# Performance work log

Hardware: AMD Instinct MI355X
Metric: run time of the kernel (lower is better)

Reference implementation:

```python
import jax, jax.numpy as jnp
import numpy as np

N_PRED = 10000
N_GT = 1000
NUM_CLASSES = 80
IMG_H = 800
IMG_W = 1333
EPS = 1e-12
ALPHA, GAMMA, CLS_W = 0.25, 2.0, 2.0
L1_W, IOU_W = 5.0, 2.0
CENTER_RADIUS = 2.5
CAND_TOPK = 5


def _make_boxes(key, n, w, h):
    k1, k2 = jax.random.split(key)
    cxcy = jax.random.uniform(k1, (n, 2)) * jnp.array([w, h], jnp.float32)
    wh = jax.random.uniform(k2, (n, 2)) * 190.0 + 10.0
    return jnp.concatenate([cxcy - wh / 2, cxcy + wh / 2], axis=1).astype(jnp.float32)


def setup_inputs() -> dict:
    key = jax.random.key(0)
    k1, k2, k3, k4 = jax.random.split(key, 4)
    return {
        'pred_logits': jax.random.normal(k1, (N_PRED, NUM_CLASSES), jnp.float32),
        'pred_boxes': _make_boxes(k2, N_PRED, IMG_W, IMG_H),
        'gt_bboxes': _make_boxes(k3, N_GT, IMG_W, IMG_H),
        'gt_labels': jax.random.randint(k4, (N_GT,), 0, NUM_CLASSES),
        'img_h': IMG_H,
        'img_w': IMG_W,
    }


def _pairwise_iou_giou(pred, gt):
    area_p = (pred[:, 2] - pred[:, 0]) * (pred[:, 3] - pred[:, 1])
    area_g = (gt[:, 2] - gt[:, 0]) * (gt[:, 3] - gt[:, 1])
    lt = jnp.maximum(pred[:, None, :2], gt[None, :, :2])
    rb = jnp.minimum(pred[:, None, 2:], gt[None, :, 2:])
    wh = jnp.clip(rb - lt, 0.0)
    inter = wh[..., 0] * wh[..., 1]                       # [N,G]
    union = area_p[:, None] + area_g[None, :] - inter
    iou = inter / jnp.maximum(union, EPS)
    elt = jnp.minimum(pred[:, None, :2], gt[None, :, :2])
    erb = jnp.maximum(pred[:, None, 2:], gt[None, :, 2:])
    ewh = jnp.clip(erb - elt, 0.0)
    enclose = ewh[..., 0] * ewh[..., 1]
    giou = iou - (enclose - union) / jnp.maximum(enclose, EPS)
    return iou, giou


def _center_info(pred, gt):
    # pred/gt in xyxy; uses pred box centers, strict inequalities as in source
    pcx = (pred[:, 0] + pred[:, 2]) * 0.5
    pcy = (pred[:, 1] + pred[:, 3]) * 0.5
    gx1, gy1, gx2, gy2 = gt[:, 0], gt[:, 1], gt[:, 2], gt[:, 3]
    in_boxes = ((pcx[:, None] > gx1) & (pcx[:, None] < gx2) &
                (pcy[:, None] > gy1) & (pcy[:, None] < gy2))
    gcx, gcy = (gx1 + gx2) * 0.5, (gy1 + gy2) * 0.5
    gw, gh = gx2 - gx1, gy2 - gy1
    r = CENTER_RADIUS
    in_centers = ((pcx[:, None] > gcx - r * gw) & (pcx[:, None] < gcx + r * gw) &
                  (pcy[:, None] > gcy - r * gh) & (pcy[:, None] < gcy + r * gh))
    valid = in_boxes.any(1) | in_centers.any(1)
    return valid, in_boxes & in_centers


def _compute_cost_and_ious(pred_logits, pred_boxes, gt_bboxes, gt_labels, img_h, img_w):
    # FocalLossCost
    p = jax.nn.sigmoid(pred_logits)
    neg = -jnp.log1p(-(p - EPS)) * (1 - ALPHA) * p ** GAMMA
    pos = -jnp.log(p + EPS) * ALPHA * (1 - p) ** GAMMA
    cls_cost = (pos - neg)[:, gt_labels] * CLS_W            # [N,G]
    # BBoxL1Cost (normalized by image size)
    factor = jnp.array([img_w, img_h, img_w, img_h], jnp.float32)
    l1_cost = jnp.sum(jnp.abs(pred_boxes[:, None, :] / factor -
                              gt_bboxes[None, :, :] / factor), -1) * L1_W
    # IoUCost (giou) + pairwise ious for dynamic-k
    ious, giou = _pairwise_iou_giou(pred_boxes, gt_bboxes)
    iou_cost = -giou * IOU_W
    valid_mask, in_boxes_and_center = _center_info(pred_boxes, gt_bboxes)
    cost = cls_cost + l1_cost + iou_cost + jnp.where(in_boxes_and_center, 0.0, 100.0)
    cost = cost + jnp.where(valid_mask, 0.0, 10000.0)[:, None]
    return cost, ious


def _dynamic_k_matching(cost, ious):
    n, g = cost.shape
    k = min(CAND_TOPK, n)
    topk_ious, _ = jax.lax.top_k(ious.T, k)                 # [G,k]
    dynamic_ks = jnp.maximum(topk_ious.sum(1).astype(jnp.int32), 1)
    _, idx = jax.lax.top_k(-cost.T, k)                      # [G,k] smallest costs per gt
    vals = (jnp.arange(k)[None, :] < dynamic_ks[:, None]).astype(cost.dtype)
    cols = jnp.broadcast_to(jnp.arange(g)[:, None], (g, k))
    mm = jnp.zeros_like(cost).at[idx, cols].max(vals)       # scatter 1s per gt column
    # resolve priors matched to >1 gt (note: mask is reused stale inside the loop, as in source)
    prior_mask = mm.sum(1) > 1
    cmin = jnp.argmin(cost, axis=1)
    mm = jnp.where(prior_mask[:, None], jax.nn.one_hot(cmin, g, dtype=cost.dtype), mm)

    def cond(state):
        m, _ = state
        return jnp.any(m.sum(0) == 0)

    def body(state):
        m, c = state
        matched_q = m.sum(1) > 0
        c = c + 100000.0 * matched_q[:, None].astype(c.dtype)
        unmatched = m.sum(0) == 0
        pos = jnp.argmin(c, axis=0)                         # [G]
        oh = jax.nn.one_hot(pos, n, dtype=c.dtype).T        # [N,G]
        m = jnp.where(unmatched[None, :], oh, m)
        cmin2 = jnp.argmin(c, axis=1)
        m_fix = jnp.where(prior_mask[:, None], jax.nn.one_hot(cmin2, g, dtype=c.dtype), m)
        m = jnp.where(jnp.any(m.sum(1) > 1), m_fix, m)
        return (m, c)

    mm, _ = jax.lax.while_loop(cond, body, (mm, cost))
    fg_mask = mm.sum(1) > 0
    matched = jnp.argmax(mm, axis=1).astype(jnp.int32)
    return fg_mask, jnp.where(fg_mask, matched, 0)


def reference(pred_logits, pred_boxes, gt_bboxes, gt_labels, img_h, img_w):
    cost, ious = _compute_cost_and_ious(pred_logits, pred_boxes, gt_bboxes,
                                        gt_labels, img_h, img_w)
    fg_mask, matched_gt = _dynamic_k_matching(cost, ious)
    # dense form: matched_gt[i] valid only where fg_mask[i] (fixed-shape version of
    # the original's compressed matched_gt_inds = mm[fg_mask].argmax(1))
    return fg_mask, matched_gt
```

## Files before the change

kernel.cpp:

```cpp
#include <hip/hip_runtime.h>
#include <cfloat>
#include <cmath>

#define NP 10000
#define NG 1000
#define NC 80
#define LMAX 6
#define NCH 4
#define CHSZ (NP / NCH)
#define CMAIN 9
#define CTAIL 196

#define S_MULTI 12
#define S_BODY  16
#define RI_BIG  0x3fffffff
#define KMAX    0xFFFFFFFFFFFFFFFFull

#define TKEY    0xC248000000000000ull

#define WCAP    448

__device__ __forceinline__ bool lexless(float av, int ai, float bv, int bi) {
    return (av < bv) || (av == bv && ai < bi);
}

__device__ __forceinline__ unsigned long long packkey(float v, int idx) {
    unsigned u = __float_as_uint(v);
    u ^= (unsigned)(((int)u) >> 31) | 0x80000000u;
    return ((unsigned long long)u << 32) | (unsigned)idx;
}
__device__ __forceinline__ int keyidx(unsigned long long k) {
    return (int)(unsigned)(k & 0xFFFFFFFFu);
}

__device__ __forceinline__ float inflate(float c, int k) {
    for (int q = 0; q < k; q++) c += 100000.0f;
    return c;
}

__device__ __forceinline__ void cost_iou(float4 p, float4 pn, float4 pi,
        float4 g, float4 cb, float4 Gn, float ga, float clsv,
        float& cc_out, float& iou_out) {
#pragma clang fp contract(off)
    float wx = fminf(p.z, g.z) - fmaxf(p.x, g.x); wx = fmaxf(wx, 0.0f);
    float wy = fminf(p.w, g.w) - fmaxf(p.y, g.y); wy = fmaxf(wy, 0.0f);
    float inter = wx * wy;
    float uni = pi.z + ga - inter;
    float iou = inter / fmaxf(uni, 1e-12f);
    float ex = fmaxf(p.z, g.z) - fminf(p.x, g.x); ex = fmaxf(ex, 0.0f);
    float ey = fmaxf(p.w, g.w) - fminf(p.y, g.y); ey = fmaxf(ey, 0.0f);
    float enc = ex * ey;
    float giou = iou - (enc - uni) / fmaxf(enc, 1e-12f);
    float l1 = ((fabsf(pn.x - Gn.x) + fabsf(pn.y - Gn.y))
                + fabsf(pn.z - Gn.z)) + fabsf(pn.w - Gn.w);
    float cc = clsv + l1 * 5.0f;
    cc = cc + (-giou * 2.0f);
    bool inb = (pi.x > g.x && pi.x < g.z && pi.y > g.y && pi.y < g.w);
    bool inc = (pi.x > cb.x && pi.x < cb.z && pi.y > cb.y && pi.y < cb.w);
    cc = cc + ((inb && inc) ? 0.0f : 100.0f);
    cc = cc + pi.w;
    cc_out = cc; iou_out = iou;
}

__device__ __forceinline__ void ins5k(unsigned long long* kv,
        unsigned long long key) {
    if (key < kv[4]) {
        kv[4] = key;
#pragma unroll
        for (int t = 4; t > 0; t--)
            if (kv[t] < kv[t-1]) { unsigned long long tv = kv[t]; kv[t] = kv[t-1]; kv[t-1] = tv; }
    }
}
__device__ __forceinline__ void ins5i(float* iv, float iou) {
    if (iou > iv[4]) {
        iv[4] = iou;
#pragma unroll
        for (int t = 4; t > 0; t--)
            if (iv[t] > iv[t-1]) { float tv = iv[t]; iv[t] = iv[t-1]; iv[t-1] = tv; }
    }
}

#define CLS_TI 64
#define PB_CLS0 40
#define PB_G0   197
#define PB_V0   201
__global__ __launch_bounds__(256) void k_prep(const float* __restrict__ logits,
        const float* __restrict__ pb, const float* __restrict__ gb,
        const int* __restrict__ imgw, const int* __restrict__ imgh,
        float* __restrict__ clsval, float4* __restrict__ pnorm,
        float4* __restrict__ pinfo, float4* __restrict__ gcb,
        float4* __restrict__ gnm, float* __restrict__ gar,
        int* rowcnt, int* rowfirst, int* rowiter, int* prior, int* priorcol,
        int* colsum, int* scal)
{
    __shared__ float sl[CLS_TI * (NC + 1)];
    int b = blockIdx.x;
    if (b < PB_CLS0) {
        int i = b * 256 + threadIdx.x;
        if (i < NP) {
            rowcnt[i] = 0; rowfirst[i] = 0x7fffffff; rowiter[i] = RI_BIG;
            prior[i] = 0; priorcol[i] = 0;
        }
        if (i < NG) colsum[i] = 0;
        if (i < 32) scal[i] = 0;
    } else if (b < PB_G0) {
        int i0 = (b - PB_CLS0) * CLS_TI;
        bool full = (i0 + CLS_TI) <= NP;
        if (full) {
            const float* src = logits + (size_t)i0 * NC;
            for (int e = threadIdx.x; e < CLS_TI * NC; e += 256) {
                int di = e / NC, c = e - di * NC;
                sl[di * (NC + 1) + c] = src[e];
            }
        } else {
            for (int e = threadIdx.x; e < CLS_TI * NC; e += 256) {
                int di = e / NC, c = e - di * NC;
                int i = i0 + di;
                sl[di * (NC + 1) + c] = (i < NP) ? logits[(size_t)i * NC + c] : 0.0f;
            }
        }
        __syncthreads();
        for (int e = threadIdx.x; e < CLS_TI * NC; e += 256) {
            int c = e >> 6, di = e & 63;
            int i = i0 + di;
            if (i >= NP) continue;
            float x = sl[di * (NC + 1) + c];
            float p = 1.0f / (1.0f + expf(-x));
            float neg = -log1pf(-(p - 1e-12f)) * 0.75f * (p * p);
            float om = 1.0f - p;
            float pos = -logf(p + 1e-12f) * 0.25f * (om * om);
            clsval[(size_t)c * NP + i] = (pos - neg) * 2.0f;
        }
    } else if (b < PB_V0) {
#pragma clang fp contract(off)
        int j = (b - PB_G0) * 256 + threadIdx.x;
        if (j < NG) {
            float fw = (float)imgw[0], fh = (float)imgh[0];
            float4 g = ((const float4*)gb)[j];
            float gcx = (g.x + g.z) * 0.5f, gcy = (g.y + g.w) * 0.5f;
            float gw = g.z - g.x, gh = g.w - g.y;
            float4 cb; cb.x = gcx - 2.5f * gw; cb.y = gcy - 2.5f * gh;
            cb.z = gcx + 2.5f * gw; cb.w = gcy + 2.5f * gh;
            gcb[j] = cb;
            float4 Gn; Gn.x = g.x / fw; Gn.y = g.y / fh; Gn.z = g.z / fw; Gn.w = g.w / fh;
            gnm[j] = Gn;
            gar[j] = (g.z - g.x) * (g.w - g.y);
        }
    } else {
#pragma clang fp contract(off)
        int wave = threadIdx.x >> 6;
        int lane = threadIdx.x & 63;
        int i = (b - PB_V0) * 4 + wave;
        if (i >= NP) return;
        float4 p = ((const float4*)pb)[i];
        float pcx = (p.x + p.z) * 0.5f, pcy = (p.y + p.w) * 0.5f;
        int vb = 0, vc = 0;
        const float4* gb4 = (const float4*)gb;
        for (int jb = 0; jb < NG; jb += 64) {
            int j = jb + lane;
            if (j < NG) {
                float4 g = gb4[j];
                vb |= (pcx > g.x && pcx < g.z && pcy > g.y && pcy < g.w) ? 1 : 0;
                float gcx = (g.x + g.z) * 0.5f, gcy = (g.y + g.w) * 0.5f;
                float gw = g.z - g.x, gh = g.w - g.y;
                vc |= (pcx > gcx - 2.5f * gw && pcx < gcx + 2.5f * gw &&
                       pcy > gcy - 2.5f * gh && pcy < gcy + 2.5f * gh) ? 1 : 0;
            }
            if (__any(vb | vc)) break;
        }
        int any = __any(vb | vc) ? 1 : 0;
        if (lane == 0) {
            float fw = (float)imgw[0], fh = (float)imgh[0];
            float4 pn; pn.x = p.x / fw; pn.y = p.y / fh; pn.z = p.z / fw; pn.w = p.w / fh;
            pnorm[i] = pn;
            float4 pi4; pi4.x = pcx; pi4.y = pcy;
            pi4.z = (p.z - p.x) * (p.w - p.y);
            pi4.w = any ? 0.0f : 10000.0f;
            pinfo[i] = pi4;
        }
    }
}

__device__ __forceinline__ void tree57(unsigned long long* s_k, float* s_iv,
        int tid) {
    for (int w = 128; w > 0; w >>= 1) {
        if (tid < w) {
            int a = tid * 7, bb = (tid + w) * 7;
            unsigned long long ok[5]; float og[5];
            int pa = a, pbp = bb;
#pragma unroll
            for (int t = 0; t < 5; t++) {
                unsigned long long A = s_k[pa], B = s_k[pbp];
                if (A <= B) { ok[t] = A; pa++; } else { ok[t] = B; pbp++; }
            }
            int qa = a, qb = bb;
#pragma unroll
            for (int t = 0; t < 5; t++) {
                float A = s_iv[qa], B = s_iv[qb];
                if (A >= B) { og[t] = A; qa++; } else { og[t] = B; qb++; }
            }
#pragma unroll
            for (int t = 0; t < 5; t++) { s_k[a+t] = ok[t]; s_iv[a+t] = og[t]; }
        }
        __syncthreads();
    }
}

__global__ __launch_bounds__(256) void k_cost2(
        const float* __restrict__ pb, const float* __restrict__ gb,
        const int* __restrict__ glab, const float* __restrict__ clsval,
        const float4* __restrict__ pnorm, const float4* __restrict__ pinfo,
        const float4* __restrict__ gcb, const float4* __restrict__ gnm,
        const float* __restrict__ gar,
        unsigned long long* __restrict__ pck, float* __restrict__ piv)
{
    __shared__ unsigned long long s_k[256 * 7];
    __shared__ float s_iv[256 * 7];
    __shared__ int s_wcnt[4];
    int* s_list = (int*)s_iv;

    int j = blockIdx.x >> 2;
    int c = blockIdx.x & 3;
    int tid = threadIdx.x;
    int wid = tid >> 6;
    int ln  = tid & 63;
    float4 g  = ((const float4*)gb)[j];
    float4 cb = gcb[j];
    float4 Gn = gnm[j];
    float  ga = gar[j];
    const float* clscol = clsval + (size_t)glab[j] * NP;
    const float4* pb4 = (const float4*)pb;
    int base_i = c * CHSZ;

    int wbase = 0;
    for (int k = 0; k <= CMAIN; k++) {
        if (k == CMAIN && tid >= CTAIL) break;
        int i = base_i + tid + k * 256;
        float4 p = pb4[i];
        bool o = (p.z > g.x) & (g.z > p.x) & (p.w > g.y) & (g.w > p.y);
        unsigned long long m = __ballot(o ? 1 : 0);
        if (o) {
            int slot = wbase + __popcll(m & ((1ull << ln) - 1ull));
            if (slot < WCAP) s_list[wid * WCAP + slot] = i;
        }
        wbase += __popcll(m);
    }
    if (ln == 0) s_wcnt[wid] = wbase;
    __syncthreads();
    int c0 = s_wcnt[0], c1 = s_wcnt[1], c2 = s_wcnt[2], c3 = s_wcnt[3];
    bool overflow = (c0 > WCAP) | (c1 > WCAP) | (c2 > WCAP) | (c3 > WCAP);

    unsigned long long kv[5]; float iv[5];
#pragma unroll
    for (int t = 0; t < 5; t++) { kv[t] = KMAX; iv[t] = overflow ? -1.0f : 0.0f; }

    if (!overflow) {
        for (int q = tid; q < c0; q += 256) {
            int i = s_list[q];
            float cc, iou;
            cost_iou(pb4[i], pnorm[i], pinfo[i], g, cb, Gn, ga, clscol[i], cc, iou);
            ins5k(kv, packkey(cc, i)); ins5i(iv, iou);
        }
        for (int q = tid; q < c1; q += 256) {
            int i = s_list[WCAP + q];
            float cc, iou;
            cost_iou(pb4[i], pnorm[i], pinfo[i], g, cb, Gn, ga, clscol[i], cc, iou);
            ins5k(kv, packkey(cc, i)); ins5i(iv, iou);
        }
        for (int q = tid; q < c2; q += 256) {
            int i = s_list[2 * WCAP + q];
            float cc, iou;
            cost_iou(pb4[i], pnorm[i], pinfo[i], g, cb, Gn, ga, clscol[i], cc, iou);
            ins5k(kv, packkey(cc, i)); ins5i(iv, iou);
        }
        for (int q = tid; q < c3; q += 256) {
            int i = s_list[3 * WCAP + q];
            float cc, iou;
            cost_iou(pb4[i], pnorm[i], pinfo[i], g, cb, Gn, ga, clscol[i], cc, iou);
            ins5k(kv, packkey(cc, i)); ins5i(iv, iou);
        }
    } else {
        for (int k = 0; k <= CMAIN; k++) {
            if (k == CMAIN && tid >= CTAIL) break;
            int i = base_i + tid + k * 256;
            float cc, iou;
            cost_iou(pb4[i], pnorm[i], pinfo[i], g, cb, Gn, ga, clscol[i], cc, iou);
            ins5k(kv, packkey(cc, i)); ins5i(iv, iou);
        }
    }
    __syncthreads();

    int base = tid * 7;
#pragma unroll
    for (int t = 0; t < 5; t++) { s_k[base+t] = kv[t]; s_iv[base+t] = iv[t]; }
    s_k[base+5] = KMAX; s_iv[base+5] = -2.0f;
    __syncthreads();
    tree57(s_k, s_iv, tid);

    bool redo = !overflow && (s_k[4] >= TKEY);
    __syncthreads();

    if (redo) {
#pragma unroll
        for (int t = 0; t < 5; t++) { kv[t] = KMAX; iv[t] = -1.0f; }
        for (int k = 0; k <= CMAIN; k++) {
            if (k == CMAIN && tid >= CTAIL) break;
            int i = base_i + tid + k * 256;
            float cc, iou;
            cost_iou(pb4[i], pnorm[i], pinfo[i], g, cb, Gn, ga, clscol[i], cc, iou);
            ins5k(kv, packkey(cc, i)); ins5i(iv, iou);
        }
#pragma unroll
        for (int t = 0; t < 5; t++) { s_k[base+t] = kv[t]; s_iv[base+t] = iv[t]; }
        s_k[base+5] = KMAX; s_iv[base+5] = -2.0f;
        __syncthreads();
        tree57(s_k, s_iv, tid);
    }

    if (tid == 0) {
        int ob = blockIdx.x * 5;
#pragma unroll
        for (int t = 0; t < 5; t++) { pck[ob + t] = s_k[t]; piv[ob + t] = s_iv[t]; }
    }
}

__global__ __launch_bounds__(256) void k_costmerge(
        const unsigned long long* __restrict__ pck, const float* __restrict__ piv,
        int* __restrict__ rowcnt, int* __restrict__ rowfirst,
        int* __restrict__ rowiter, int* __restrict__ top5,
        int* __restrict__ dkarr)
{
    int j = blockIdx.x * 256 + threadIdx.x;
    if (j >= NG) return;
    int base = j * NCH * 5;
    int h0 = 0, h1 = 0, h2 = 0, h3 = 0;
    int besti[5];
#pragma unroll
    for (int r = 0; r < 5; r++) {
        unsigned long long v0 = (h0 < 5) ? pck[base + h0]      : KMAX;
        unsigned long long v1 = (h1 < 5) ? pck[base + 5 + h1]  : KMAX;
        unsigned long long v2 = (h2 < 5) ? pck[base + 10 + h2] : KMAX;
        unsigned long long v3 = (h3 < 5) ? pck[base + 15 + h3] : KMAX;
        unsigned long long best = v0; int sel = 0;
        if (v1 < best) { best = v1; sel = 1; }
        if (v2 < best) { best = v2; sel = 2; }
        if (v3 < best) { best = v3; sel = 3; }
        besti[r] = keyidx(best);
        h0 += (sel == 0); h1 += (sel == 1); h2 += (sel == 2); h3 += (sel == 3);
    }
    int g0 = 0, g1 = 0, g2 = 0, g3 = 0;
    float ivm[5];
#pragma unroll
    for (int r = 0; r < 5; r++) {
        float w0 = (g0 < 5) ? piv[base + g0]      : -2.0f;
        float w1 = (g1 < 5) ? piv[base + 5 + g1]  : -2.0f;
        float w2 = (g2 < 5) ? piv[base + 10 + g2] : -2.0f;
        float w3 = (g3 < 5) ? piv[base + 15 + g3] : -2.0f;
        float best = w0; int sel = 0;
        if (w1 > best) { best = w1; sel = 1; }
        if (w2 > best) { best = w2; sel = 2; }
        if (w3 > best) { best = w3; sel = 3; }
        ivm[r] = best;
        g0 += (sel == 0); g1 += (sel == 1); g2 += (sel == 2); g3 += (sel == 3);
    }
    float s = (((ivm[0] + ivm[1]) + ivm[2]) + ivm[3]) + ivm[4];
    int dk = (int)s;
    if (dk < 1) dk = 1;
    dkarr[j] = dk;
#pragma unroll
    for (int r = 0; r < 5; r++) top5[j * 5 + r] = besti[r];
    for (int t = 0; t < dk; t++) {
        int r = besti[t];
        atomicAdd(&rowcnt[r], 1);
        atomicMin(&rowfirst[r], j);
        atomicMin(&rowiter[r], -1);
    }
}

__global__ __launch_bounds__(256) void k_pfixsurv(const float* __restrict__ pb,
        const float* __restrict__ gb, const int* __restrict__ glab,
        const float* __restrict__ clsval,
        const float4* __restrict__ pnorm, const float4* __restrict__ pinfo,
        const float4* __restrict__ gcb, const float4* __restrict__ gnm,
        const float* __restrict__ gar,
        int* __restrict__ prior, int* __restrict__ priorcol,
        int* __restrict__ colsum,
        const int* __restrict__ rowcnt, const int* __restrict__ top5,
        const int* __restrict__ dkarr)
{
    int b = blockIdx.x;
    int tid = threadIdx.x;
    if (b >= 2500) {
        int j = (b - 2500) * 256 + tid;
        if (j >= NG) return;
        int c = 0;
        int dk = dkarr[j];
        for (int t = 0; t < dk; t++) if (rowcnt[top5[j * 5 + t]] == 1) c++;
        if (c) atomicAdd(&colsum[j], c);
        return;
    }
    __shared__ float rv[256]; __shared__ int ri[256];
    for (int q = 0; q < 4; q++) {
        int row = b * 4 + q;
        if (rowcnt[row] <= 1) continue;
        if (tid == 0) prior[row] = 1;
        float4 p = ((const float4*)pb)[row];
        float4 pn = pnorm[row];
        float4 pi4 = pinfo[row];
        float best = FLT_MAX; int bj = 0x7fffffff;
        for (int j = tid; j < NG; j += 256) {
            float cc, iou;
            cost_iou(p, pn, pi4, ((const float4*)gb)[j], gcb[j], gnm[j], gar[j],
                     clsval[(size_t)glab[j] * NP + row], cc, iou);
            if (lexless(cc, j, best, bj)) { best = cc; bj = j; }
        }
        rv[tid] = best; ri[tid] = bj; __syncthreads();
        for (int w = 128; w > 0; w >>= 1) {
            if (tid < w) {
                float ov = rv[tid + w]; int oi = ri[tid + w];
                if (lexless(ov, oi, rv[tid], ri[tid])) { rv[tid] = ov; ri[tid] = oi; }
            }
            __syncthreads();
        }
        if (tid == 0) {
            priorcol[row] = ri[0];
            atomicAdd(&colsum[ri[0]], 1);
        }
        __syncthreads();
    }
}

__global__ __launch_bounds__(256) void k_iterB(const float* __restrict__ pb,
        const float* __restrict__ gb, const int* __restrict__ glab,
        const float* __restrict__ clsval,
        const float4* __restrict__ pnorm, const float4* __restrict__ pinfo,
        const float4* __restrict__ gcb, const float4* __restrict__ gnm,
        const float* __restrict__ gar, const int* __restrict__ top5,
        int* __restrict__ rowiter, int* __restrict__ rowcnt,
        int* __restrict__ rowfirst, int* __restrict__ colsum,
        int* __restrict__ scal, int t)
{
    int j = blockIdx.x;
    if (colsum[j] != 0) return;
    int tid = threadIdx.x;
    if (tid == 0) scal[S_BODY + t] = 1;

    __shared__ int s_pos;
    if (tid == 0) {
        int pos = -1;
        for (int r = 0; r < 5; r++) {
            int i = top5[j * 5 + r];
            if (rowiter[i] >= t) { pos = i; break; }
        }
        s_pos = pos;
    }
    __syncthreads();
    int pos = s_pos;

    if (pos < 0) {
        float4 g  = ((const float4*)gb)[j];
        float4 cb = gcb[j];
        float4 Gn = gnm[j];
        float  ga = gar[j];
        const float* clscol = clsval + (size_t)glab[j] * NP;
        const float4* pb4 = (const float4*)pb;
        __shared__ float rv[256]; __shared__ int ri[256];
        float best = FLT_MAX; int bi = 0x7fffffff;
        for (int i = tid; i < NP; i += 256) {
            if (rowiter[i] < t) continue;
            float cc, iou;
            cost_iou(pb4[i], pnorm[i], pinfo[i], g, cb, Gn, ga, clscol[i], cc, iou);
            if (lexless(cc, i, best, bi)) { best = cc; bi = i; }
        }
        rv[tid] = best; ri[tid] = bi; __syncthreads();
        for (int w = 128; w > 0; w >>= 1) {
            if (tid < w) {
                float ov = rv[tid + w]; int oi = ri[tid + w];
                if (lexless(ov, oi, rv[tid], ri[tid])) { rv[tid] = ov; ri[tid] = oi; }
            }
            __syncthreads();
        }
        pos = ri[0];
    }

    if (tid == 0) {
        colsum[j] = 1;
        int old = atomicAdd(&rowcnt[pos], 1);
        if (old >= 1) scal[S_MULTI] = 1;
        atomicMin(&rowfirst[pos], j);
        atomicMin(&rowiter[pos], t);
    }
}

__global__ __launch_bounds__(256) void k_iterC(const float* __restrict__ pb,
        const float* __restrict__ gb, const int* __restrict__ glab,
        const float* __restrict__ clsval,
        const float4* __restrict__ pnorm, const float4* __restrict__ pinfo,
        const float4* __restrict__ gcb, const float4* __restrict__ gnm,
        const float* __restrict__ gar,
        const int* __restrict__ prior, const int* __restrict__ rowiter,
        int* __restrict__ priorcol, int* __restrict__ colsum,
        int* __restrict__ scal, int t)
{
    if (scal[S_BODY + t] == 0 || scal[S_MULTI] == 0) return;
    int b = blockIdx.x;
    int tid = threadIdx.x;
    __shared__ float rv[256]; __shared__ int ri[256];
    for (int q = 0; q < 4; q++) {
        int row = b * 4 + q;
        if (!prior[row]) continue;
        int k = t - rowiter[row]; if (k < 0) k = 0;
        float4 p = ((const float4*)pb)[row];
        float4 pn = pnorm[row];
        float4 pi4 = pinfo[row];
        float best = FLT_MAX; int bj = 0x7fffffff;
        for (int j = tid; j < NG; j += 256) {
            float cc, iou;
            cost_iou(p, pn, pi4, ((const float4*)gb)[j], gcb[j], gnm[j], gar[j],
                     clsval[(size_t)glab[j] * NP + row], cc, iou);
            float val = inflate(cc, k);
            if (lexless(val, j, best, bj)) { best = val; bj = j; }
        }
        rv[tid] = best; ri[tid] = bj; __syncthreads();
        for (int w = 128; w > 0; w >>= 1) {
            if (tid < w) {
                float ov = rv[tid + w]; int oi = ri[tid + w];
                if (lexless(ov, oi, rv[tid], ri[tid])) { rv[tid] = ov; ri[tid] = oi; }
            }
            __syncthreads();
        }
        if (tid == 0) {
            int nb = ri[0];
            int oldc = priorcol[row];
            if (nb != oldc) {
                atomicSub(&colsum[oldc], 1);
                atomicAdd(&colsum[nb], 1);
                priorcol[row] = nb;
            }
        }
        __syncthreads();
    }
}

__global__ __launch_bounds__(256) void k_final(const int* __restrict__ rowcnt,
        const int* __restrict__ prior, const int* __restrict__ priorcol,
        const int* __restrict__ rowfirst, int* __restrict__ out)
{
    int i = blockIdx.x * 256 + threadIdx.x;
    if (i >= NP) return;
    int fg = rowcnt[i] > 0;
    out[i] = fg ? 1 : 0;
    out[NP + i] = fg ? (prior[i] ? priorcol[i] : rowfirst[i]) : 0;
}

extern "C" void kernel_launch(void* const* d_in, const int* in_sizes, int n_in,
                              void* d_out, int out_size, void* d_ws, size_t ws_size,
                              hipStream_t stream)
{
    (void)in_sizes; (void)n_in; (void)out_size; (void)ws_size;
    const float* logits = (const float*)d_in[0];
    const float* pboxes = (const float*)d_in[1];
    const float* gboxes = (const float*)d_in[2];
    const int*   glab   = (const int*)d_in[3];
    const int*   imgh   = (const int*)d_in[4];
    const int*   imgw   = (const int*)d_in[5];
    int* out = (int*)d_out;

    char* w = (char*)d_ws;
    float*  clsval  = (float*)(w);
    float4* pnorm   = (float4*)(w + 3200000);
    float4* pinfo   = (float4*)(w + 3360000);
    float4* gcb     = (float4*)(w + 3520000);
    float4* gnm     = (float4*)(w + 3536000);
    float*  gar     = (float*)(w + 3552000);
    int* rowcnt     = (int*)(w + 3556000);
    int* rowfirst   = (int*)(w + 3596000);
    int* rowiter    = (int*)(w + 3636000);
    int* prior      = (int*)(w + 3676000);
    int* priorcol   = (int*)(w + 3716000);
    int* top5       = (int*)(w + 3756000);
    int* dkarr      = (int*)(w + 3776000);
    int* colsum     = (int*)(w + 3780000);
    int* scal       = (int*)(w + 3784000);
    unsigned long long* pck = (unsigned long long*)(w + 3784128);
    float* piv      = (float*)(w + 3944128);

    hipLaunchKernelGGL(k_prep, dim3(2701), dim3(256), 0, stream,
                       logits, pboxes, gboxes, imgw, imgh,
                       clsval, pnorm, pinfo, gcb, gnm, gar,
                       rowcnt, rowfirst, rowiter, prior, priorcol, colsum, scal);
    hipLaunchKernelGGL(k_cost2, dim3(NG * NCH), dim3(256), 0, stream,
                       pboxes, gboxes, glab, clsval, pnorm, pinfo, gcb, gnm, gar,
                       pck, piv);
    hipLaunchKernelGGL(k_costmerge, dim3(4), dim3(256), 0, stream,
                       pck, piv, rowcnt, rowfirst, rowiter, top5, dkarr);
    hipLaunchKernelGGL(k_pfixsurv, dim3(2504), dim3(256), 0, stream,
                       pboxes, gboxes, glab, clsval, pnorm, pinfo, gcb, gnm, gar,
                       prior, priorcol, colsum, rowcnt, top5, dkarr);
    for (int t = 0; t < LMAX; t++) {
        hipLaunchKernelGGL(k_iterB, dim3(NG), dim3(256), 0, stream,
                           pboxes, gboxes, glab, clsval, pnorm, pinfo, gcb, gnm, gar,
                           top5, rowiter, rowcnt, rowfirst, colsum, scal, t);
        hipLaunchKernelGGL(k_iterC, dim3(2500), dim3(256), 0, stream,
                           pboxes, gboxes, glab, clsval, pnorm, pinfo, gcb, gnm, gar,
                           prior, rowiter, priorcol, colsum, scal, t);
    }
    hipLaunchKernelGGL(k_final, dim3(40), dim3(256), 0, stream,
                       rowcnt, prior, priorcol, rowfirst, out);
}
```

Measured before the change: 163.1 us.

## Assign each wave one prediction chunk and merge top-5 via wave shuffles

The cost kernel now launches one block per ground-truth box, and each of the four waves independently handles one quarter of the predictions. This replaces the four-blocks-per-GT scheme. The shared-memory tree merge with many __syncthreads is replaced by a butterfly shuffle merge of sorted top-5 lists within each wave, and the per-wave candidate list capacity is raised. The intent is to remove block-wide barriers and shared-memory traffic. In exchange, each wave scans four times as many boxes serially and the grid has fewer blocks.

```diff
diff --git a/kernel.cpp b/kernel.cpp
--- a/kernel.cpp
+++ b/kernel.cpp
@@ -8,8 +8,8 @@
 #define LMAX 6
 #define NCH 4
 #define CHSZ (NP / NCH)
-#define CMAIN 9
-#define CTAIL 196
+#define WMAIN 39
+#define WTAIL 4
 
 #define S_MULTI 12
 #define S_BODY  16
@@ -18,7 +18,7 @@
 
 #define TKEY    0xC248000000000000ull
 
-#define WCAP    448
+#define WCAP    768
 
 __device__ __forceinline__ bool lexless(float av, int ai, float bv, int bi) {
     return (av < bv) || (av == bv && ai < bi);
@@ -80,6 +80,55 @@
     }
 }
 
+__device__ __forceinline__ void cswapk(unsigned long long& a,
+        unsigned long long& b) {
+    unsigned long long lo = (a < b) ? a : b;
+    unsigned long long hi = (a < b) ? b : a;
+    a = lo; b = hi;
+}
+__device__ __forceinline__ void sort5k(unsigned long long* a) {
+    cswapk(a[0],a[1]); cswapk(a[3],a[4]); cswapk(a[2],a[4]);
+    cswapk(a[2],a[3]); cswapk(a[1],a[4]); cswapk(a[0],a[3]);
+    cswapk(a[0],a[2]); cswapk(a[1],a[3]); cswapk(a[1],a[2]);
+}
+__device__ __forceinline__ void cswapi(float& a, float& b) {
+    float hi = fmaxf(a, b), lo = fminf(a, b);
+    a = hi; b = lo;
+}
+__device__ __forceinline__ void sort5i(float* a) {
+    cswapi(a[0],a[1]); cswapi(a[3],a[4]); cswapi(a[2],a[4]);
+    cswapi(a[2],a[3]); cswapi(a[1],a[4]); cswapi(a[0],a[3]);
+    cswapi(a[0],a[2]); cswapi(a[1],a[3]); cswapi(a[1],a[2]);
+}
+
+__device__ __forceinline__ void wavemerge5(unsigned long long* kv, float* iv) {
+#pragma unroll
+    for (int d = 1; d < 64; d <<= 1) {
+        unsigned long long r0 = __shfl_xor(kv[0], d);
+        unsigned long long r1 = __shfl_xor(kv[1], d);
+        unsigned long long r2 = __shfl_xor(kv[2], d);
+        unsigned long long r3 = __shfl_xor(kv[3], d);
+        unsigned long long r4 = __shfl_xor(kv[4], d);
+        kv[0] = (kv[0] < r4) ? kv[0] : r4;
+        kv[1] = (kv[1] < r3) ? kv[1] : r3;
+        kv[2] = (kv[2] < r2) ? kv[2] : r2;
+        kv[3] = (kv[3] < r1) ? kv[3] : r1;
+        kv[4] = (kv[4] < r0) ? kv[4] : r0;
+        sort5k(kv);
+        float s0 = __shfl_xor(iv[0], d);
+        float s1 = __shfl_xor(iv[1], d);
+        float s2 = __shfl_xor(iv[2], d);
+        float s3 = __shfl_xor(iv[3], d);
+        float s4 = __shfl_xor(iv[4], d);
+        iv[0] = fmaxf(iv[0], s4);
+        iv[1] = fmaxf(iv[1], s3);
+        iv[2] = fmaxf(iv[2], s2);
+        iv[3] = fmaxf(iv[3], s1);
+        iv[4] = fmaxf(iv[4], s0);
+        sort5i(iv);
+    }
+}
+
 #define CLS_TI 64
 #define PB_CLS0 40
 #define PB_G0   197
@@ -181,31 +230,6 @@
     }
 }
 
-__device__ __forceinline__ void tree57(unsigned long long* s_k, float* s_iv,
-        int tid) {
-    for (int w = 128; w > 0; w >>= 1) {
-        if (tid < w) {
-            int a = tid * 7, bb = (tid + w) * 7;
-            unsigned long long ok[5]; float og[5];
-            int pa = a, pbp = bb;
-#pragma unroll
-            for (int t = 0; t < 5; t++) {
-                unsigned long long A = s_k[pa], B = s_k[pbp];
-                if (A <= B) { ok[t] = A; pa++; } else { ok[t] = B; pbp++; }
-            }
-            int qa = a, qb = bb;
-#pragma unroll
-            for (int t = 0; t < 5; t++) {
-                float A = s_iv[qa], B = s_iv[qb];
-                if (A >= B) { og[t] = A; qa++; } else { og[t] = B; qb++; }
-            }
-#pragma unroll
-            for (int t = 0; t < 5; t++) { s_k[a+t] = ok[t]; s_iv[a+t] = og[t]; }
-        }
-        __syncthreads();
-    }
-}
-
 __global__ __launch_bounds__(256) void k_cost2(
         const float* __restrict__ pb, const float* __restrict__ gb,
         const int* __restrict__ glab, const float* __restrict__ clsval,
@@ -214,13 +238,9 @@
         const float* __restrict__ gar,
         unsigned long long* __restrict__ pck, float* __restrict__ piv)
 {
-    __shared__ unsigned long long s_k[256 * 7];
-    __shared__ float s_iv[256 * 7];
-    __shared__ int s_wcnt[4];
-    int* s_list = (int*)s_iv;
-
-    int j = blockIdx.x >> 2;
-    int c = blockIdx.x & 3;
+    __shared__ int s_list[4 * WCAP];
+
+    int j = blockIdx.x;
     int tid = threadIdx.x;
     int wid = tid >> 6;
     int ln  = tid & 63;
@@ -230,14 +250,14 @@
     float  ga = gar[j];
     const float* clscol = clsval + (size_t)glab[j] * NP;
     const float4* pb4 = (const float4*)pb;
-    int base_i = c * CHSZ;
+    int base_i = wid * CHSZ;
 
     int wbase = 0;
-    for (int k = 0; k <= CMAIN; k++) {
-        if (k == CMAIN && tid >= CTAIL) break;
-        int i = base_i + tid + k * 256;
-        float4 p = pb4[i];
-        bool o = (p.z > g.x) & (g.z > p.x) & (p.w > g.y) & (g.w > p.y);
+    for (int k = 0; k <= WMAIN; k++) {
+        bool valid = (k < WMAIN) | (ln < WTAIL);
+        int i = base_i + ln + k * 64;
+        float4 p = pb4[valid ? i : base_i];
+        bool o = valid & (p.z > g.x) & (g.z > p.x) & (p.w > g.y) & (g.w > p.y);
         unsigned long long m = __ballot(o ? 1 : 0);
         if (o) {
             int slot = wbase + __popcll(m & ((1ull << ln) - 1ull));
@@ -245,82 +265,53 @@
         }
         wbase += __popcll(m);
     }
-    if (ln == 0) s_wcnt[wid] = wbase;
-    __syncthreads();
-    int c0 = s_wcnt[0], c1 = s_wcnt[1], c2 = s_wcnt[2], c3 = s_wcnt[3];
-    bool overflow = (c0 > WCAP) | (c1 > WCAP) | (c2 > WCAP) | (c3 > WCAP);
+    int cnt = wbase;
+    bool overflow = (cnt > WCAP);
 
     unsigned long long kv[5]; float iv[5];
 #pragma unroll
     for (int t = 0; t < 5; t++) { kv[t] = KMAX; iv[t] = overflow ? -1.0f : 0.0f; }
 
     if (!overflow) {
-        for (int q = tid; q < c0; q += 256) {
-            int i = s_list[q];
+        for (int q = ln; q < cnt; q += 64) {
+            int i = s_list[wid * WCAP + q];
             float cc, iou;
             cost_iou(pb4[i], pnorm[i], pinfo[i], g, cb, Gn, ga, clscol[i], cc, iou);
             ins5k(kv, packkey(cc, i)); ins5i(iv, iou);
         }
-        for (int q = tid; q < c1; q += 256) {
-            int i = s_list[WCAP + q];
-            float cc, iou;
-            cost_iou(pb4[i], pnorm[i], pinfo[i], g, cb, Gn, ga, clscol[i], cc, iou);
-            ins5k(kv, packkey(cc, i)); ins5i(iv, iou);
-        }
-        for (int q = tid; q < c2; q += 256) {
-            int i = s_list[2 * WCAP + q];
-            float cc, iou;
-            cost_iou(pb4[i], pnorm[i], pinfo[i], g, cb, Gn, ga, clscol[i], cc, iou);
-            ins5k(kv, packkey(cc, i)); ins5i(iv, iou);
-        }
-        for (int q = tid; q < c3; q += 256) {
-            int i = s_list[3 * WCAP + q];
-            float cc, iou;
-            cost_iou(pb4[i], pnorm[i], pinfo[i], g, cb, Gn, ga, clscol[i], cc, iou);
-            ins5k(kv, packkey(cc, i)); ins5i(iv, iou);
-        }
     } else {
-        for (int k = 0; k <= CMAIN; k++) {
-            if (k == CMAIN && tid >= CTAIL) break;
-            int i = base_i + tid + k * 256;
-            float cc, iou;
-            cost_iou(pb4[i], pnorm[i], pinfo[i], g, cb, Gn, ga, clscol[i], cc, iou);
-            ins5k(kv, packkey(cc, i)); ins5i(iv, iou);
-        }
-    }
-    __syncthreads();
-
-    int base = tid * 7;
-#pragma unroll
-    for (int t = 0; t < 5; t++) { s_k[base+t] = kv[t]; s_iv[base+t] = iv[t]; }
-    s_k[base+5] = KMAX; s_iv[base+5] = -2.0f;
-    __syncthreads();
-    tree57(s_k, s_iv, tid);
-
-    bool redo = !overflow && (s_k[4] >= TKEY);
-    __syncthreads();
-
+        for (int k = 0; k <= WMAIN; k++) {
+            bool valid = (k < WMAIN) | (ln < WTAIL);
+            if (valid) {
+                int i = base_i + ln + k * 64;
+                float cc, iou;
+                cost_iou(pb4[i], pnorm[i], pinfo[i], g, cb, Gn, ga, clscol[i], cc, iou);
+                ins5k(kv, packkey(cc, i)); ins5i(iv, iou);
+            }
+        }
+    }
+    wavemerge5(kv, iv);
+
+    bool redo = !overflow && (kv[4] >= TKEY);
     if (redo) {
 #pragma unroll
         for (int t = 0; t < 5; t++) { kv[t] = KMAX; iv[t] = -1.0f; }
-        for (int k = 0; k <= CMAIN; k++) {
-            if (k == CMAIN && tid >= CTAIL) break;
-            int i = base_i + tid + k * 256;
-            float cc, iou;
-            cost_iou(pb4[i], pnorm[i], pinfo[i], g, cb, Gn, ga, clscol[i], cc, iou);
-            ins5k(kv, packkey(cc, i)); ins5i(iv, iou);
-        }
-#pragma unroll
-        for (int t = 0; t < 5; t++) { s_k[base+t] = kv[t]; s_iv[base+t] = iv[t]; }
-        s_k[base+5] = KMAX; s_iv[base+5] = -2.0f;
-        __syncthreads();
-        tree57(s_k, s_iv, tid);
-    }
-
-    if (tid == 0) {
-        int ob = blockIdx.x * 5;
-#pragma unroll
-        for (int t = 0; t < 5; t++) { pck[ob + t] = s_k[t]; piv[ob + t] = s_iv[t]; }
+        for (int k = 0; k <= WMAIN; k++) {
+            bool valid = (k < WMAIN) | (ln < WTAIL);
+            if (valid) {
+                int i = base_i + ln + k * 64;
+                float cc, iou;
+                cost_iou(pb4[i], pnorm[i], pinfo[i], g, cb, Gn, ga, clscol[i], cc, iou);
+                ins5k(kv, packkey(cc, i)); ins5i(iv, iou);
+            }
+        }
+        wavemerge5(kv, iv);
+    }
+
+    if (ln == 0) {
+        int ob = (j * NCH + wid) * 5;
+#pragma unroll
+        for (int t = 0; t < 5; t++) { pck[ob + t] = kv[t]; piv[ob + t] = iv[t]; }
     }
 }
 
@@ -589,7 +580,7 @@
                        logits, pboxes, gboxes, imgw, imgh,
                        clsval, pnorm, pinfo, gcb, gnm, gar,
                        rowcnt, rowfirst, rowiter, prior, priorcol, colsum, scal);
-    hipLaunchKernelGGL(k_cost2, dim3(NG * NCH), dim3(256), 0, stream,
+    hipLaunchKernelGGL(k_cost2, dim3(NG), dim3(256), 0, stream,
                        pboxes, gboxes, glab, clsval, pnorm, pinfo, gcb, gnm, gar,
                        pck, piv);
     hipLaunchKernelGGL(k_costmerge, dim3(4), dim3(256), 0, stream,
```

New measurement: 166.6 us. 2.1% more time.
